# Performance work log

Hardware: AMD Instinct MI355X
Metric: run time of the kernel (lower is better)

The kernel has to match this reference:

```python
import jax, jax.numpy as jnp
import numpy as np

Q_DIM = 1024
K_DIM = 1024
V_DIM = 1024
ATTEN_DIM = 1024
NUM_HEADS = 16
HEAD_DIM = ATTEN_DIM // NUM_HEADS
B, L = 4, 2048


def setup_inputs() -> dict:
    key = jax.random.key(0)
    ks = jax.random.split(key, 11)
    s = 0.02
    return {
        "query": jax.random.normal(ks[0], (B, L, Q_DIM), dtype=jnp.float32),
        "key":   jax.random.normal(ks[1], (B, L, K_DIM), dtype=jnp.float32),
        "value": jax.random.normal(ks[2], (B, L, V_DIM), dtype=jnp.float32),
        "Wq": jax.random.normal(ks[3], (Q_DIM, ATTEN_DIM), dtype=jnp.float32) * s,
        "bq": jnp.zeros((ATTEN_DIM,), dtype=jnp.float32),
        "Wk": jax.random.normal(ks[4], (K_DIM, ATTEN_DIM), dtype=jnp.float32) * s,
        "bk": jnp.zeros((ATTEN_DIM,), dtype=jnp.float32),
        "Wv": jax.random.normal(ks[5], (V_DIM, ATTEN_DIM), dtype=jnp.float32) * s,
        "bv": jnp.zeros((ATTEN_DIM,), dtype=jnp.float32),
        "Wo": jax.random.normal(ks[6], (ATTEN_DIM, V_DIM), dtype=jnp.float32) * s,
        "bo": jnp.zeros((V_DIM,), dtype=jnp.float32),
    }


def reference(query, key, value, Wq, bq, Wk, bk, Wv, bv, Wo, bo):
    # QKV projections
    q = query @ Wq + bq        # [B, L, A]
    k = key   @ Wk + bk        # [B, L, A]
    v = value @ Wv + bv        # [B, L, A]
    # split heads: [B, L, H, D]
    def split_heads(x):
        return x.reshape(x.shape[:-1] + (NUM_HEADS, HEAD_DIM))
    q, k, v = split_heads(q), split_heads(k), split_heads(v)
    scale = 1.0 / (HEAD_DIM ** 0.5)
    # scores: [B, H, Lq, Lk]
    scores = jnp.einsum("bqhd,bkhd->bhqk", q, k) * scale
    attn = jax.nn.softmax(scores, axis=-1)
    out = jnp.einsum("bhqk,bkhd->bqhd", attn, v)  # [B, Lq, H, D]
    out = out.reshape(out.shape[0], out.shape[1], ATTEN_DIM)
    return out @ Wo + bo
```

## Files before the change

kernel.cpp:

```cpp
#include <hip/hip_runtime.h>
#include <stdint.h>

#define L_SEQ 2048
#define BATCH 4
#define ADIM  1024
#define NH    16
#define HD    64

typedef __attribute__((ext_vector_type(8))) short bf16x8;
typedef __attribute__((ext_vector_type(4))) float f32x4;
typedef __attribute__((ext_vector_type(16))) float f32x16;
typedef __attribute__((ext_vector_type(2))) int i32x2;

__device__ __forceinline__ short f2bf(float f) {
    union { float f; unsigned u; } x; x.f = f;
    unsigned r = x.u + 0x7fffu + ((x.u >> 16) & 1u);
    return (short)(r >> 16);
}

__device__ __forceinline__ void async_ld16(void* lds, const void* g) {
    __builtin_amdgcn_global_load_lds(
        (const __attribute__((address_space(1))) void*)g,
        (__attribute__((address_space(3))) void*)lds, 16, 0, 0);
}

__device__ __forceinline__ int cvtpk_bf16(float a, float b) {
    int r;
    asm("v_cvt_pk_bf16_f32 %0, %1, %2" : "=v"(r) : "v"(a), "v"(b));
    return r;
}

__device__ __forceinline__ bf16x8 pack4(int a, int b, int c, int d) {
    union { int i[4]; bf16x8 v; } u;
    u.i[0] = a; u.i[1] = b; u.i[2] = c; u.i[3] = d;
    return u.v;
}

__global__ void cvt3_kernel(const float* __restrict__ s0, const float* __restrict__ s1,
                            const float* __restrict__ s2, short* __restrict__ dst, int n4) {
    int i = blockIdx.x * blockDim.x + threadIdx.x;
    if (i >= n4) return;
    int z = blockIdx.y;
    const float* src = (z == 0) ? s0 : (z == 1) ? s1 : s2;
    float4 v = reinterpret_cast<const float4*>(src)[i];
    short4 s;
    s.x = f2bf(v.x); s.y = f2bf(v.y); s.z = f2bf(v.z); s.w = f2bf(v.w);
    reinterpret_cast<short4*>(dst + (size_t)z * (BATCH * L_SEQ * ADIM))[i] = s;
}

__global__ void transpose4_kernel(const float* __restrict__ W0, const float* __restrict__ W1,
                                  const float* __restrict__ W2, const float* __restrict__ W3,
                                  short* __restrict__ outb) {
    __shared__ float t[32][33];
    int z = blockIdx.z;
    const float* in = (z == 0) ? W0 : (z == 1) ? W1 : (z == 2) ? W2 : W3;
    short* out = outb + (size_t)z * (ADIM * ADIM);
    int x  = blockIdx.x * 32 + threadIdx.x;
    int y0 = blockIdx.y * 32 + threadIdx.y;
#pragma unroll
    for (int j = 0; j < 4; ++j)
        t[threadIdx.y + 8 * j][threadIdx.x] = in[(y0 + 8 * j) * 1024 + x];
    __syncthreads();
    int x2 = blockIdx.y * 32 + threadIdx.x;
    int y2 = blockIdx.x * 32 + threadIdx.y;
#pragma unroll
    for (int j = 0; j < 4; ++j)
        out[(y2 + 8 * j) * 1024 + x2] = f2bf(t[threadIdx.x][threadIdx.y + 8 * j]);
}

__device__ __forceinline__ void gemm_core(const short* __restrict__ A,
                                          const short* __restrict__ BT,
                                          const float* __restrict__ bias,
                                          void* __restrict__ Cout,
                                          int mode, float scalemul) {
    const int K = 1024, N = 1024;
    __shared__ __align__(16) short As[128 * 32];
    __shared__ __align__(16) short Bs[128 * 32];
    int tid = threadIdx.x;
    int wave = tid >> 6, lane = tid & 63, quad = lane >> 4, l16 = lane & 15;
    int wm = wave & 1, wn = wave >> 1;
    int m0 = blockIdx.y * 128, n0 = blockIdx.x * 128;
    f32x4 acc[4][4] = {};

    int row = tid >> 2, ck = tid & 3;
    const short* gA0 = A  + (size_t)(m0 + row) * K + ck * 8;
    const short* gA1 = gA0 + (size_t)64 * K;
    const short* gB0 = BT + (size_t)(n0 + row) * K + ck * 8;
    const short* gB1 = gB0 + (size_t)64 * K;
    short* lA0 = As + tid * 8;  short* lA1 = As + tid * 8 + 2048;
    short* lB0 = Bs + tid * 8;  short* lB1 = Bs + tid * 8 + 2048;

    for (int kb = 0; kb < K; kb += 32) {
        async_ld16(lA0, gA0); async_ld16(lA1, gA1);
        async_ld16(lB0, gB0); async_ld16(lB1, gB1);
        gA0 += 32; gA1 += 32; gB0 += 32; gB1 += 32;
        __syncthreads();
        bf16x8 af[4], bf[4];
#pragma unroll
        for (int mt = 0; mt < 4; ++mt)
            af[mt] = *(const bf16x8*)&As[(wm * 64 + mt * 16 + l16) * 32 + quad * 8];
#pragma unroll
        for (int nt = 0; nt < 4; ++nt)
            bf[nt] = *(const bf16x8*)&Bs[(wn * 64 + nt * 16 + l16) * 32 + quad * 8];
#pragma unroll
        for (int mt = 0; mt < 4; ++mt)
#pragma unroll
            for (int nt = 0; nt < 4; ++nt)
                acc[mt][nt] = __builtin_amdgcn_mfma_f32_16x16x32_bf16(
                    af[mt], bf[nt], acc[mt][nt], 0, 0, 0);
        __syncthreads();
    }

    if (mode == 0) {
#pragma unroll
        for (int nt = 0; nt < 4; ++nt) {
            int col = n0 + wn * 64 + nt * 16 + l16;
            float bv = bias[col];
#pragma unroll
            for (int mt = 0; mt < 4; ++mt)
#pragma unroll
                for (int r = 0; r < 4; ++r) {
                    int rw = m0 + wm * 64 + mt * 16 + quad * 4 + r;
                    ((short*)Cout)[(size_t)rw * N + col] = f2bf((acc[mt][nt][r] + bv) * scalemul);
                }
        }
    } else if (mode == 1) {
#pragma unroll
        for (int nt = 0; nt < 4; ++nt) {
            int col = n0 + wn * 64 + nt * 16 + l16;
            float bv = bias[col];
            int h = col >> 6, d = col & 63;
#pragma unroll
            for (int mt = 0; mt < 4; ++mt)
#pragma unroll
                for (int r = 0; r < 4; ++r) {
                    int rw = m0 + wm * 64 + mt * 16 + quad * 4 + r;
                    int b = rw >> 11, lk = rw & 2047;
                    ((short*)Cout)[(((size_t)b * NH + h) * HD + d) * L_SEQ + lk] =
                        f2bf(acc[mt][nt][r] + bv);
                }
        }
    } else {
#pragma unroll
        for (int nt = 0; nt < 4; ++nt) {
            int col = n0 + wn * 64 + nt * 16 + l16;
            float bv = bias[col];
#pragma unroll
            for (int mt = 0; mt < 4; ++mt)
#pragma unroll
                for (int r = 0; r < 4; ++r) {
                    int rw = m0 + wm * 64 + mt * 16 + quad * 4 + r;
                    ((float*)Cout)[(size_t)rw * N + col] = acc[mt][nt][r] + bv;
                }
        }
    }
}

__global__ __launch_bounds__(256)
void gemm_one(const short* __restrict__ A, const short* __restrict__ BT,
              const float* __restrict__ bias, void* __restrict__ Cout,
              int mode, float scalemul) {
    gemm_core(A, BT, bias, Cout, mode, scalemul);
}

__global__ __launch_bounds__(256)
void qkv_gemm(const short* __restrict__ Xbase, const short* __restrict__ WTbase,
              const float* __restrict__ bq, const float* __restrict__ bk,
              const float* __restrict__ bv,
              short* __restrict__ Qb, short* __restrict__ Kb, short* __restrict__ VTout,
              float qscale) {
    int z = blockIdx.z;
    const short* A  = Xbase + (size_t)z * (BATCH * L_SEQ * ADIM);
    const short* BT = WTbase + (size_t)z * (ADIM * ADIM);
    const float* bias = (z == 0) ? bq : (z == 1) ? bk : bv;
    void* out = (z == 0) ? (void*)Qb : (z == 1) ? (void*)Kb : (void*)VTout;
    int mode = (z == 2) ? 1 : 0;
    float sm = (z == 0) ? qscale : 1.0f;
    gemm_core(A, BT, bias, out, mode, sm);
}

__global__ __launch_bounds__(256, 4)
void attn_kernel(const short* __restrict__ Qb, const short* __restrict__ Kb,
                 const short* __restrict__ VT, short* __restrict__ Oout) {
    __shared__ __align__(16) short lds[16384];
    int tid = threadIdx.x;
    int wave = tid >> 6, lane = tid & 63;
    int r31 = lane & 31, hi = lane >> 5;
    int h = blockIdx.y, b = blockIdx.z;

    size_t qrow = (size_t)(b * L_SEQ + blockIdx.x * 128 + wave * 32 + r31) * ADIM + h * HD;
    bf16x8 qf[4];
#pragma unroll
    for (int dc = 0; dc < 4; ++dc)
        qf[dc] = *(const bf16x8*)&Qb[qrow + dc * 16 + hi * 8];

    const short* Kbase = Kb + (size_t)b * L_SEQ * ADIM + h * HD;
    const short* Vbase = VT + ((size_t)(b * NH + h) * HD) * L_SEQ;
    const short* gp[4]; int step[4]; int ldso[4];
#pragma unroll
    for (int s = 0; s < 4; ++s) {
        int j = s * 256 + tid;
        ldso[s] = j * 8;
        if (j < 512) {
            int row = j >> 3, c = (j & 7) ^ (row & 7);
            gp[s] = Kbase + (size_t)row * ADIM + c * 8;
            step[s] = 64 * ADIM;
        } else {
            int jv = j - 512;
            int row = jv >> 3, c = (jv & 7) ^ (row & 7);
            gp[s] = Vbase + (size_t)row * L_SEQ + c * 8;
            step[s] = 64;
        }
    }

    f32x16 o0 = {}, o1 = {};
    f32x4 lp = {};

#pragma unroll
    for (int s = 0; s < 4; ++s) { async_ld16(lds + ldso[s], gp[s]); gp[s] += step[s]; }
    __syncthreads();

    int cur = 0;
    for (int t = 0; t < 32; ++t) {
        const short* kb_l = lds + cur * 8192;
        const short* vb_l = kb_l + 4096;
        if (t < 31) {
            short* dst = lds + (cur ^ 1) * 8192;
#pragma unroll
            for (int s = 0; s < 4; ++s) { async_ld16(dst + ldso[s], gp[s]); gp[s] += step[s]; }
        }
#pragma unroll
        for (int kt = 0; kt < 2; ++kt) {
            const short* krow = kb_l + (kt * 32 + r31) * 64;
            f32x16 sv = {};
#pragma unroll
            for (int dc = 0; dc < 4; ++dc) {
                bf16x8 kf = *(const bf16x8*)&krow[((((dc << 1) + hi) ^ (r31 & 7)) << 3)];
                sv = __builtin_amdgcn_mfma_f32_32x32x16_bf16(kf, qf[dc], sv, 0, 0, 0);
            }
#pragma unroll
            for (int r = 0; r < 16; ++r) sv[r] = __builtin_amdgcn_exp2f(sv[r]);
#pragma unroll
            for (int m = 0; m < 4; ++m)
#pragma unroll
                for (int j2 = 0; j2 < 4; ++j2) lp[j2] += sv[m * 4 + j2];

            int p0 = cvtpk_bf16(sv[0],  sv[1]);
            int p1 = cvtpk_bf16(sv[2],  sv[3]);
            int p2 = cvtpk_bf16(sv[4],  sv[5]);
            int p3 = cvtpk_bf16(sv[6],  sv[7]);
            int p4 = cvtpk_bf16(sv[8],  sv[9]);
            int p5 = cvtpk_bf16(sv[10], sv[11]);
            int p6 = cvtpk_bf16(sv[12], sv[13]);
            int p7 = cvtpk_bf16(sv[14], sv[15]);
            asm volatile("v_permlane32_swap_b32 %0, %1" : "+v"(p0), "+v"(p2));
            asm volatile("v_permlane32_swap_b32 %0, %1" : "+v"(p1), "+v"(p3));
            asm volatile("v_permlane32_swap_b32 %0, %1" : "+v"(p4), "+v"(p6));
            asm volatile("v_permlane32_swap_b32 %0, %1" : "+v"(p5), "+v"(p7));
            bf16x8 pf0 = pack4(p0, p1, p2, p3);
            bf16x8 pf1 = pack4(p4, p5, p6, p7);

            const short* vrow = vb_l + r31 * 64;
#pragma unroll
            for (int dt = 0; dt < 2; ++dt) {
                const short* vr = vrow + dt * 2048;
                bf16x8 vf0 = *(const bf16x8*)&vr[((((kt << 2) + hi)     ^ (r31 & 7)) << 3)];
                bf16x8 vf1 = *(const bf16x8*)&vr[((((kt << 2) + 2 + hi) ^ (r31 & 7)) << 3)];
                if (dt == 0) {
                    o0 = __builtin_amdgcn_mfma_f32_32x32x16_bf16(vf0, pf0, o0, 0, 0, 0);
                    o0 = __builtin_amdgcn_mfma_f32_32x32x16_bf16(vf1, pf1, o0, 0, 0, 0);
                } else {
                    o1 = __builtin_amdgcn_mfma_f32_32x32x16_bf16(vf0, pf0, o1, 0, 0, 0);
                    o1 = __builtin_amdgcn_mfma_f32_32x32x16_bf16(vf1, pf1, o1, 0, 0, 0);
                }
            }
        }
        __syncthreads();
        cur ^= 1;
    }

    float lsum = lp[0] + lp[1] + lp[2] + lp[3];
    lsum += __shfl_xor(lsum, 32);
    float inv = __builtin_amdgcn_rcpf(lsum);

    short* tile = lds + wave * (32 * 68);
#pragma unroll
    for (int dt = 0; dt < 2; ++dt)
#pragma unroll
        for (int g = 0; g < 4; ++g) {
            int d0 = dt * 32 + g * 8 + hi * 4;
            int pa, pb;
            if (dt == 0) {
                pa = cvtpk_bf16(o0[g * 4 + 0] * inv, o0[g * 4 + 1] * inv);
                pb = cvtpk_bf16(o0[g * 4 + 2] * inv, o0[g * 4 + 3] * inv);
            } else {
                pa = cvtpk_bf16(o1[g * 4 + 0] * inv, o1[g * 4 + 1] * inv);
                pb = cvtpk_bf16(o1[g * 4 + 2] * inv, o1[g * 4 + 3] * inv);
            }
            *(i32x2*)&tile[r31 * 68 + d0] = (i32x2){pa, pb};
        }
    __syncthreads();
    size_t obase = (size_t)(b * L_SEQ + blockIdx.x * 128 + wave * 32) * ADIM + h * HD;
    int rr = lane >> 3, cc = lane & 7;
#pragma unroll
    for (int p = 0; p < 4; ++p) {
        int row = p * 8 + rr;
        bf16x8 v = *(const bf16x8*)&tile[row * 68 + cc * 8];
        *(bf16x8*)&Oout[obase + (size_t)row * ADIM + cc * 8] = v;
    }
}

extern "C" void kernel_launch(void* const* d_in, const int* in_sizes, int n_in,
                              void* d_out, int out_size, void* d_ws, size_t ws_size,
                              hipStream_t stream) {
    const float* query = (const float*)d_in[0];
    const float* keyp  = (const float*)d_in[1];
    const float* value = (const float*)d_in[2];
    const float* Wq = (const float*)d_in[3];
    const float* bq = (const float*)d_in[4];
    const float* Wk = (const float*)d_in[5];
    const float* bk = (const float*)d_in[6];
    const float* Wv = (const float*)d_in[7];
    const float* bv = (const float*)d_in[8];
    const float* Wo = (const float*)d_in[9];
    const float* bo = (const float*)d_in[10];

    const float QSCALE = 0.125f * 1.44269504f;
    const size_t MB = 1ull << 20;
    const int n4 = (BATCH * L_SEQ * ADIM) / 4;
    char* w = (char*)d_ws;
    dim3 tblk(32, 8);
    dim3 gemm_grid(ADIM / 128, (BATCH * L_SEQ) / 128);
    dim3 attn_grid(L_SEQ / 128, NH, BATCH);

    if (ws_size >= 104 * MB) {
        short* X0  = (short*)(w);
        short* WT  = (short*)(w + 48 * MB);
        short* VT  = (short*)(w + 56 * MB);
        short* Kb  = (short*)(w + 72 * MB);
        short* Qb  = (short*)(w + 88 * MB);
        short* AO  = X0;

        cvt3_kernel<<<dim3(n4 / 256, 3), 256, 0, stream>>>(query, keyp, value, X0, n4);
        transpose4_kernel<<<dim3(32, 32, 4), tblk, 0, stream>>>(Wq, Wk, Wv, Wo, WT);
        qkv_gemm<<<dim3(ADIM / 128, (BATCH * L_SEQ) / 128, 3), 256, 0, stream>>>(
            X0, WT, bq, bk, bv, Qb, Kb, VT, QSCALE);
        attn_kernel<<<attn_grid, 256, 0, stream>>>(Qb, Kb, VT, AO);
        gemm_one<<<gemm_grid, 256, 0, stream>>>(AO, WT + (size_t)3 * ADIM * ADIM, bo,
                                                d_out, 2, 1.0f);
    } else {
        short* X0  = (short*)(w);
        short* WT  = (short*)(w + 16 * MB);
        short* VT  = (short*)(w + 24 * MB);
        short* Kb  = (short*)(w + 40 * MB);
        short* Qb  = (short*)(w + 56 * MB);

        transpose4_kernel<<<dim3(32, 32, 4), tblk, 0, stream>>>(Wq, Wk, Wv, Wo, WT);
        cvt3_kernel<<<dim3(n4 / 256, 1), 256, 0, stream>>>(query, query, query, X0, n4);
        gemm_one<<<gemm_grid, 256, 0, stream>>>(X0, WT, bq, Qb, 0, QSCALE);
        cvt3_kernel<<<dim3(n4 / 256, 1), 256, 0, stream>>>(keyp, keyp, keyp, X0, n4);
        gemm_one<<<gemm_grid, 256, 0, stream>>>(X0, WT + (size_t)ADIM * ADIM, bk, Kb, 0, 1.0f);
        cvt3_kernel<<<dim3(n4 / 256, 1), 256, 0, stream>>>(value, value, value, X0, n4);
        gemm_one<<<gemm_grid, 256, 0, stream>>>(X0, WT + (size_t)2 * ADIM * ADIM, bv, VT, 1, 1.0f);
        attn_kernel<<<attn_grid, 256, 0, stream>>>(Qb, Kb, VT, X0);
        gemm_one<<<gemm_grid, 256, 0, stream>>>(X0, WT + (size_t)3 * ADIM * ADIM, bo,
                                                d_out, 2, 1.0f);
    }
}
```

Measured before the change: 356.7 us.

## Double-buffer GEMM LDS tiles and swizzle block order for XCD locality

The GEMM core now uses a two-stage LDS buffer, issuing the async global-to-LDS loads for the next K-slice before computing on the current one, so there is one barrier per iteration instead of two and load latency overlaps MFMA work. Both GEMM kernels and the attention kernel remap block IDs with an XCD-aware swizzle (stride 8), so blocks sharing A or K/V tiles land on the same chiplet's L2. GEMM launch bounds now request 4 blocks per CU. The price is twice the GEMM LDS (32 KB per block), which together with the register cap may limit occupancy or cause spills.

New measurement: 341.8 us. 1.04x faster.

```diff
diff --git a/kernel.cpp b/kernel.cpp
--- a/kernel.cpp
+++ b/kernel.cpp
@@ -72,14 +72,13 @@
                                           const short* __restrict__ BT,
                                           const float* __restrict__ bias,
                                           void* __restrict__ Cout,
-                                          int mode, float scalemul) {
+                                          int mode, float scalemul,
+                                          int m0, int n0) {
     const int K = 1024, N = 1024;
-    __shared__ __align__(16) short As[128 * 32];
-    __shared__ __align__(16) short Bs[128 * 32];
+    __shared__ __align__(16) short smem[16384];
     int tid = threadIdx.x;
     int wave = tid >> 6, lane = tid & 63, quad = lane >> 4, l16 = lane & 15;
     int wm = wave & 1, wn = wave >> 1;
-    int m0 = blockIdx.y * 128, n0 = blockIdx.x * 128;
     f32x4 acc[4][4] = {};
 
     int row = tid >> 2, ck = tid & 3;
@@ -87,28 +86,39 @@
     const short* gA1 = gA0 + (size_t)64 * K;
     const short* gB0 = BT + (size_t)(n0 + row) * K + ck * 8;
     const short* gB1 = gB0 + (size_t)64 * K;
-    short* lA0 = As + tid * 8;  short* lA1 = As + tid * 8 + 2048;
-    short* lB0 = Bs + tid * 8;  short* lB1 = Bs + tid * 8 + 2048;
-
-    for (int kb = 0; kb < K; kb += 32) {
-        async_ld16(lA0, gA0); async_ld16(lA1, gA1);
-        async_ld16(lB0, gB0); async_ld16(lB1, gB1);
-        gA0 += 32; gA1 += 32; gB0 += 32; gB1 += 32;
-        __syncthreads();
-        bf16x8 af[4], bf[4];
+    int loA0 = tid * 8, loA1 = tid * 8 + 2048;
+    int loB0 = tid * 8 + 4096, loB1 = tid * 8 + 6144;
+
+    async_ld16(smem + loA0, gA0); async_ld16(smem + loA1, gA1);
+    async_ld16(smem + loB0, gB0); async_ld16(smem + loB1, gB1);
+    gA0 += 32; gA1 += 32; gB0 += 32; gB1 += 32;
+    __syncthreads();
+
+    int cur = 0;
+    for (int t = 0; t < 32; ++t) {
+        if (t < 31) {
+            int off = (cur ^ 1) * 8192;
+            async_ld16(smem + off + loA0, gA0); async_ld16(smem + off + loA1, gA1);
+            async_ld16(smem + off + loB0, gB0); async_ld16(smem + off + loB1, gB1);
+            gA0 += 32; gA1 += 32; gB0 += 32; gB1 += 32;
+        }
+        const short* Ab = smem + cur * 8192;
+        const short* Bb = Ab + 4096;
+        bf16x8 af[4], bfr[4];
 #pragma unroll
         for (int mt = 0; mt < 4; ++mt)
-            af[mt] = *(const bf16x8*)&As[(wm * 64 + mt * 16 + l16) * 32 + quad * 8];
+            af[mt] = *(const bf16x8*)&Ab[(wm * 64 + mt * 16 + l16) * 32 + quad * 8];
 #pragma unroll
         for (int nt = 0; nt < 4; ++nt)
-            bf[nt] = *(const bf16x8*)&Bs[(wn * 64 + nt * 16 + l16) * 32 + quad * 8];
+            bfr[nt] = *(const bf16x8*)&Bb[(wn * 64 + nt * 16 + l16) * 32 + quad * 8];
 #pragma unroll
         for (int mt = 0; mt < 4; ++mt)
 #pragma unroll
             for (int nt = 0; nt < 4; ++nt)
                 acc[mt][nt] = __builtin_amdgcn_mfma_f32_16x16x32_bf16(
-                    af[mt], bf[nt], acc[mt][nt], 0, 0, 0);
+                    af[mt], bfr[nt], acc[mt][nt], 0, 0, 0);
         __syncthreads();
+        cur ^= 1;
     }
 
     if (mode == 0) {
@@ -156,14 +166,22 @@
     }
 }
 
-__global__ __launch_bounds__(256)
+__device__ __forceinline__ void gemm_swz(int& m0, int& n0) {
+    int bid = blockIdx.y * 8 + blockIdx.x;
+    int swz = (bid & 7) * 64 + (bid >> 3);
+    n0 = (swz & 7) * 128;
+    m0 = (swz >> 3) * 128;
+}
+
+__global__ __launch_bounds__(256, 4)
 void gemm_one(const short* __restrict__ A, const short* __restrict__ BT,
               const float* __restrict__ bias, void* __restrict__ Cout,
               int mode, float scalemul) {
-    gemm_core(A, BT, bias, Cout, mode, scalemul);
-}
-
-__global__ __launch_bounds__(256)
+    int m0, n0; gemm_swz(m0, n0);
+    gemm_core(A, BT, bias, Cout, mode, scalemul, m0, n0);
+}
+
+__global__ __launch_bounds__(256, 4)
 void qkv_gemm(const short* __restrict__ Xbase, const short* __restrict__ WTbase,
               const float* __restrict__ bq, const float* __restrict__ bk,
               const float* __restrict__ bv,
@@ -176,7 +194,8 @@
     void* out = (z == 0) ? (void*)Qb : (z == 1) ? (void*)Kb : (void*)VTout;
     int mode = (z == 2) ? 1 : 0;
     float sm = (z == 0) ? qscale : 1.0f;
-    gemm_core(A, BT, bias, out, mode, sm);
+    int m0, n0; gemm_swz(m0, n0);
+    gemm_core(A, BT, bias, out, mode, sm, m0, n0);
 }
 
 __global__ __launch_bounds__(256, 4)
@@ -186,9 +205,14 @@
     int tid = threadIdx.x;
     int wave = tid >> 6, lane = tid & 63;
     int r31 = lane & 31, hi = lane >> 5;
-    int h = blockIdx.y, b = blockIdx.z;
-
-    size_t qrow = (size_t)(b * L_SEQ + blockIdx.x * 128 + wave * 32 + r31) * ADIM + h * HD;
+
+    int f = (blockIdx.z * NH + blockIdx.y) * (L_SEQ / 128) + blockIdx.x;
+    int swz = (f & 7) * 128 + (f >> 3);
+    int qb = swz & 15;
+    int h  = (swz >> 4) & 15;
+    int b  = swz >> 8;
+
+    size_t qrow = (size_t)(b * L_SEQ + qb * 128 + wave * 32 + r31) * ADIM + h * HD;
     bf16x8 qf[4];
 #pragma unroll
     for (int dc = 0; dc < 4; ++dc)
@@ -300,7 +324,7 @@
             *(i32x2*)&tile[r31 * 68 + d0] = (i32x2){pa, pb};
         }
     __syncthreads();
-    size_t obase = (size_t)(b * L_SEQ + blockIdx.x * 128 + wave * 32) * ADIM + h * HD;
+    size_t obase = (size_t)(b * L_SEQ + qb * 128 + wave * 32) * ADIM + h * HD;
     int rr = lane >> 3, cc = lane & 7;
 #pragma unroll
     for (int p = 0; p < 4; ++p) {
```
